# Kernel tuning notes

Hardware: AMD Instinct MI355X
Metric: run time of the kernel (lower is better)

Reference implementation:

```python
import jax, jax.numpy as jnp
import numpy as np
from functools import partial

EPS = 1e-5
TAU = 0.1

def bn(x, g, b, axes):
    m = jnp.mean(x, axis=axes, keepdims=True)
    v = jnp.var(x, axis=axes, keepdims=True)
    return (x - m) * jax.lax.rsqrt(v + EPS) * g + b

def conv(x, w, b):
    # x: NCHW, w: OIHW, stride 1, padding 1
    y = jax.lax.conv_general_dilated(x, w, (1, 1), ((1, 1), (1, 1)),
                                     dimension_numbers=('NCHW', 'OIHW', 'NCHW'))
    return y + b[None, :, None, None]

def maxpool2(x):
    return jax.lax.reduce_window(x, -jnp.inf, jax.lax.max, (1, 1, 2, 2), (1, 1, 2, 2), 'VALID')

def setup_inputs() -> dict:
    key = jax.random.key(0)
    ks = jax.random.split(key, 24)
    s = 0.02
    B = 4096
    d = {}
    d['input_data'] = jax.random.normal(ks[0], (B, 3, 32, 32), jnp.float32)
    d['conv1_w'] = jax.random.normal(ks[1], (32, 3, 3, 3), jnp.float32) * s
    d['conv1_b'] = jnp.zeros((32,), jnp.float32)
    d['bn1_g'] = jnp.ones((32,), jnp.float32); d['bn1_b'] = jnp.zeros((32,), jnp.float32)
    d['conv2_w'] = jax.random.normal(ks[2], (64, 32, 3, 3), jnp.float32) * s
    d['conv2_b'] = jnp.zeros((64,), jnp.float32)
    d['bn2_g'] = jnp.ones((64,), jnp.float32); d['bn2_b'] = jnp.zeros((64,), jnp.float32)
    d['conv3_w'] = jax.random.normal(ks[3], (128, 64, 3, 3), jnp.float32) * s
    d['conv3_b'] = jnp.zeros((128,), jnp.float32)
    d['bn3_g'] = jnp.ones((128,), jnp.float32); d['bn3_b'] = jnp.zeros((128,), jnp.float32)
    d['pre_w'] = jax.random.normal(ks[4], (1024, 8192), jnp.float32) * s
    d['pre_b'] = jnp.zeros((1024,), jnp.float32)
    d['bnp_g'] = jnp.ones((1024,), jnp.float32); d['bnp_b'] = jnp.zeros((1024,), jnp.float32)
    d['disc_w'] = jax.random.normal(ks[5], (384, 1024), jnp.float32) * s
    d['disc_b'] = jnp.zeros((384,), jnp.float32)
    d['bnd_g'] = jnp.ones((384,), jnp.float32); d['bnd_b'] = jnp.zeros((384,), jnp.float32)
    d['dfc_w'] = jax.random.normal(ks[6], (2, 384), jnp.float32) * s
    d['dfc_b'] = jnp.zeros((2,), jnp.float32)
    d['sw_w'] = jax.random.normal(ks[7], (2, 384), jnp.float32) * s
    d['sw_b'] = jnp.zeros((2,), jnp.float32)
    # partitioned classifier: P=2, Linear(1024 -> 192) + ReLU + Linear(192 -> 10)
    d['p1_w'] = jax.random.normal(ks[8], (2, 192, 1024), jnp.float32) * s
    d['p1_b'] = jnp.zeros((2, 192), jnp.float32)
    d['p2_w'] = jax.random.normal(ks[9], (2, 10, 192), jnp.float32) * s
    d['p2_b'] = jnp.zeros((2, 10), jnp.float32)
    return d

def reference(input_data, conv1_w, conv1_b, bn1_g, bn1_b, conv2_w, conv2_b, bn2_g, bn2_b,
              conv3_w, conv3_b, bn3_g, bn3_b, pre_w, pre_b, bnp_g, bnp_b,
              disc_w, disc_b, bnd_g, bnd_b, dfc_w, dfc_b, sw_w, sw_b,
              p1_w, p1_b, p2_w, p2_b):
    B = input_data.shape[0]
    # feature extractor
    x = jax.nn.relu(bn(conv(input_data, conv1_w, conv1_b), bn1_g[None, :, None, None], bn1_b[None, :, None, None], (0, 2, 3)))
    x = maxpool2(x)
    x = jax.nn.relu(bn(conv(x, conv2_w, conv2_b), bn2_g[None, :, None, None], bn2_b[None, :, None, None], (0, 2, 3)))
    x = maxpool2(x)
    x = jax.nn.relu(bn(conv(x, conv3_w, conv3_b), bn3_g[None, :, None, None], bn3_b[None, :, None, None], (0, 2, 3)))
    feat = x.reshape(B, -1)  # [B, 8192]
    feat = jax.nn.relu(bn(feat @ pre_w.T + pre_b, bnp_g[None, :], bnp_b[None, :], (0,)))  # [B, 1024]
    # discriminator branch
    dpen = jax.nn.relu(bn(feat @ disc_w.T + disc_b, bnd_g[None, :], bnd_b[None, :], (0,)))  # [B, 384]
    domain_output = dpen @ dfc_w.T + dfc_b  # [B, 2]
    sw_logits = dpen @ sw_w.T + sw_b  # [B, P]
    # gumbel-softmax (soft) + multinomial sample of partition
    key = jax.random.key(42)
    k1, k2 = jax.random.split(key)
    u = jax.random.uniform(k1, sw_logits.shape, jnp.float32, 1e-10, 1.0)
    gumbel = -jnp.log(-jnp.log(u))
    y = jax.nn.softmax((sw_logits + gumbel) / TAU, axis=-1)  # [B, P]
    partition_idx = jax.random.categorical(k2, jnp.log(y + 1e-20), axis=-1)  # [B]
    # per-partition expert MLP computed densely (P=2), then gather chosen partition
    h = jax.nn.relu(jnp.einsum('bi,poi->pbo', feat, p1_w) + p1_b[:, None, :])  # [P, B, 192]
    logits = jnp.einsum('pbo,pco->pbc', h, p2_w) + p2_b[:, None, :]  # [P, B, 10]
    sel = logits[partition_idx, jnp.arange(B)]  # [B, 10]
    # original multiplies single-element stack by full gumbel vector and sums -> scale by sum(y)=1
    class_output_partitioned = sel * jnp.sum(y, axis=1, keepdims=True)
    return (class_output_partitioned, domain_output, partition_idx)
```

## Files before the change

### kernel.cpp

```cpp
#include <hip/hip_runtime.h>
#include <cstdint>
#include <cstddef>

typedef __attribute__((ext_vector_type(8))) short short8;
typedef __attribute__((ext_vector_type(4))) float f32x4;
typedef __attribute__((ext_vector_type(16))) float f32x16;

__host__ __device__ inline void threefry2x32(uint32_t k0, uint32_t k1,
                                             uint32_t x0, uint32_t x1,
                                             uint32_t& o0, uint32_t& o1) {
  uint32_t ks2 = k0 ^ k1 ^ 0x1BD11BDAu;
  uint32_t v0 = x0 + k0, v1 = x1 + k1;
#define TF_R(r) { v0 += v1; v1 = (v1 << (r)) | (v1 >> (32 - (r))); v1 ^= v0; }
  TF_R(13) TF_R(15) TF_R(26) TF_R(6)
  v0 += k1; v1 += ks2 + 1u;
  TF_R(17) TF_R(29) TF_R(16) TF_R(24)
  v0 += ks2; v1 += k0 + 2u;
  TF_R(13) TF_R(15) TF_R(26) TF_R(6)
  v0 += k0; v1 += k1 + 3u;
  TF_R(17) TF_R(29) TF_R(16) TF_R(24)
  v0 += k1; v1 += ks2 + 4u;
  TF_R(13) TF_R(15) TF_R(26) TF_R(6)
  v0 += ks2; v1 += k0 + 5u;
#undef TF_R
  o0 = v0; o1 = v1;
}

__device__ __forceinline__ uint32_t tf_bits32(uint32_t k0, uint32_t k1, uint32_t j) {
  uint32_t o0, o1;
  threefry2x32(k0, k1, 0u, j, o0, o1);
  return o0 ^ o1;
}

__device__ __forceinline__ float u01_from_bits(uint32_t bits) {
  return __uint_as_float((bits >> 9) | 0x3f800000u) - 1.0f;
}

__device__ __forceinline__ float waveSum(float v) {
#pragma unroll
  for (int off = 32; off > 0; off >>= 1) v += __shfl_down(v, off, 64);
  return v;
}

__global__ __launch_bounds__(256) void conv1_fused_kernel(
    const float* __restrict__ in, const float* __restrict__ w,
    float* __restrict__ outraw, float* __restrict__ partials) {
  __shared__ float ins[3 * 34 * 34];
  __shared__ float red[4][64];
  const int b = blockIdx.x, t = threadIdx.x;
  for (int i = t; i < 3 * 34 * 34; i += 256) {
    int ci = i / 1156, r = i % 1156, iy = r / 34, ix = r % 34;
    int y = iy - 1, x = ix - 1;
    float v = 0.f;
    if ((unsigned)y < 32u && (unsigned)x < 32u)
      v = in[(((size_t)b * 3 + ci) * 32 + y) * 32 + x];
    ins[i] = v;
  }
  __syncthreads();
  const int py = t >> 4, px = t & 15, wv = t >> 6, ln = t & 63;
  float win[3][4][4];
#pragma unroll
  for (int ci = 0; ci < 3; ci++)
#pragma unroll
    for (int r = 0; r < 4; r++)
#pragma unroll
      for (int c = 0; c < 4; c++)
        win[ci][r][c] = ins[ci * 1156 + (2 * py + r) * 34 + (2 * px + c)];
#pragma unroll 1
  for (int co = 0; co < 32; co++) {
    float acc00 = 0.f, acc01 = 0.f, acc10 = 0.f, acc11 = 0.f;
#pragma unroll
    for (int ci = 0; ci < 3; ci++) {
      const float* wp = w + (co * 3 + ci) * 9;
#pragma unroll
      for (int dy = 0; dy < 3; dy++)
#pragma unroll
        for (int dx = 0; dx < 3; dx++) {
          float wvv = wp[dy * 3 + dx];
          acc00 += win[ci][dy][dx] * wvv;
          acc01 += win[ci][dy][dx + 1] * wvv;
          acc10 += win[ci][dy + 1][dx] * wvv;
          acc11 += win[ci][dy + 1][dx + 1] * wvv;
        }
    }
    float sm = acc00 + acc01 + acc10 + acc11;
    float sq = acc00 * acc00 + acc01 * acc01 + acc10 * acc10 + acc11 * acc11;
    float s = waveSum(sm), q = waveSum(sq);
    if (ln == 0) { red[wv][2 * co] = s; red[wv][2 * co + 1] = q; }
    float m = fmaxf(fmaxf(acc00, acc01), fmaxf(acc10, acc11));
    outraw[(((size_t)b * 32 + co) * 16 + py) * 16 + px] = m;
  }
  __syncthreads();
  for (int i = t; i < 64; i += 256)
    partials[(size_t)b * 64 + i] = red[0][i] + red[1][i] + red[2][i] + red[3][i];
}

__device__ __forceinline__ uint32_t pack_bf16q(float x) {
  uint32_t u = __float_as_uint(x);
  uint32_t hi = u & 0xffff0000u;
  float r = x - __uint_as_float(hi);
  uint32_t lo = __float_as_uint(r) >> 16;
  return hi | lo;
}

__device__ __forceinline__ uint4 pk4bn(float4 v, float sc, float sh) {
  uint4 o;
  o.x = pack_bf16q(fmaxf(v.x * sc + sh, 0.f));
  o.y = pack_bf16q(fmaxf(v.y * sc + sh, 0.f));
  o.z = pack_bf16q(fmaxf(v.z * sc + sh, 0.f));
  o.w = pack_bf16q(fmaxf(v.w * sc + sh, 0.f));
  return o;
}

__global__ void cvt_bf16q_kernel(const float* X, uint32_t* Y, int n4) {
  int i = blockIdx.x * blockDim.x + threadIdx.x;
  if (i >= n4) return;
  float4 x = ((const float4*)X)[i];
  uint4 o;
  o.x = pack_bf16q(x.x); o.y = pack_bf16q(x.y);
  o.z = pack_bf16q(x.z); o.w = pack_bf16q(x.w);
  ((uint4*)Y)[i] = o;
}

__global__ void prep_w2_kernel(const float* __restrict__ w, short* __restrict__ wh,
                               short* __restrict__ wl) {
  int idx = blockIdx.x * 256 + threadIdx.x;
  if (idx >= 64 * 32 * 9) return;
  int tp = idx % 9, rem = idx / 9;
  int ci = rem % 32, co = rem / 32;
  uint32_t pq = pack_bf16q(w[idx]);
  size_t o = ((size_t)tp * 64 + co) * 32 + ci;
  wh[o] = (short)(pq >> 16);
  wl[o] = (short)(pq & 0xffffu);
}

__global__ void prep_w3_kernel(const float* __restrict__ w, short* __restrict__ wh,
                               short* __restrict__ wl) {
  int idx = blockIdx.x * 256 + threadIdx.x;
  if (idx >= 128 * 64 * 9) return;
  int tp = idx % 9, rem = idx / 9;
  int ci = rem % 64, co = rem / 64;
  uint32_t pq = pack_bf16q(w[idx]);
  size_t o = ((size_t)tp * 128 + co) * 64 + ci;
  wh[o] = (short)(pq >> 16);
  wl[o] = (short)(pq & 0xffffu);
}

#define STORE2(ARR_H, ARR_L, ROW, KB, SW, U, V)                                 \
  {                                                                             \
    uint32_t h0 = (U.x >> 16) | (U.y & 0xffff0000u);                            \
    uint32_t h1 = (U.z >> 16) | (U.w & 0xffff0000u);                            \
    uint32_t h2 = (V.x >> 16) | (V.y & 0xffff0000u);                            \
    uint32_t h3 = (V.z >> 16) | (V.w & 0xffff0000u);                            \
    uint32_t l0 = (U.x & 0xffffu) | (U.y << 16);                                \
    uint32_t l1 = (U.z & 0xffffu) | (U.w << 16);                                \
    uint32_t l2 = (V.x & 0xffffu) | (V.y << 16);                                \
    uint32_t l3 = (V.z & 0xffffu) | (V.w << 16);                                \
    int idx = (ROW) * 32 + ((KB) ^ (SW));                                       \
    *(uint4*)&ARR_H[idx] = make_uint4(h0, h1, h2, h3);                          \
    *(uint4*)&ARR_L[idx] = make_uint4(l0, l1, l2, l3);                          \
  }

__global__ __launch_bounds__(256) void conv2_mfma_kernel(
    const float* __restrict__ in, const float* __restrict__ scale1,
    const float* __restrict__ shift1, const short* __restrict__ wh,
    const short* __restrict__ wl, float* __restrict__ outpool,
    float* __restrict__ partials) {
  __shared__ short Xh[324 * 32], Xl[324 * 32];
  __shared__ float red[4][128];
  const int b = blockIdx.x, t = threadIdx.x;
  for (int i = t; i < 324 * 16; i += 256) {
    int row = i >> 4;
    int py = row / 18, pxx = row % 18;
    if (py == 0 || py == 17 || pxx == 0 || pxx == 17) {
      ((uint32_t*)Xh)[i] = 0u;
      ((uint32_t*)Xl)[i] = 0u;
    }
  }
  for (int i = t; i < 4096; i += 256) {
    int p = i >> 8, px = i & 255;
    int y = px >> 4, x = px & 15;
    float va = in[((size_t)b * 32 + 2 * p) * 256 + px];
    float vb = in[((size_t)b * 32 + 2 * p + 1) * 256 + px];
    va = fmaxf(va * scale1[2 * p] + shift1[2 * p], 0.f);
    vb = fmaxf(vb * scale1[2 * p + 1] + shift1[2 * p + 1], 0.f);
    uint32_t ua = pack_bf16q(va), ub = pack_bf16q(vb);
    uint32_t h = (ua >> 16) | (ub & 0xffff0000u);
    uint32_t l = (ua & 0xffffu) | (ub << 16);
    int row = (y + 1) * 18 + (x + 1);
    int ci2 = (2 * p) ^ ((row & 3) << 3);
    ((uint32_t*)Xh)[(row * 32 + ci2) >> 1] = h;
    ((uint32_t*)Xl)[(row * 32 + ci2) >> 1] = l;
  }
  __syncthreads();
  const int w = t >> 6, l = t & 63;
  const int lr = l & 15, lg = l >> 4;
  f32x4 acc[4][4];
#pragma unroll
  for (int i = 0; i < 4; i++)
#pragma unroll
    for (int j = 0; j < 4; j++) acc[i][j] = (f32x4){0.f, 0.f, 0.f, 0.f};
#pragma unroll 1
  for (int tap = 0; tap < 9; tap++) {
    const int dy = tap / 3, dx = tap % 3;
    short8 awh[4], awl[4];
#pragma unroll
    for (int i = 0; i < 4; i++) {
      size_t off = ((size_t)tap * 64 + i * 16 + lr) * 32 + lg * 8;
      awh[i] = *(const short8*)(wh + off);
      awl[i] = *(const short8*)(wl + off);
    }
    short8 bxh[4], bxl[4];
#pragma unroll
    for (int j = 0; j < 4; j++) {
      int y = w * 4 + j, x = lr;
      int row = (y + dy) * 18 + (x + dx);
      int ci = (lg * 8) ^ ((row & 3) << 3);
      bxh[j] = *(const short8*)&Xh[row * 32 + ci];
      bxl[j] = *(const short8*)&Xl[row * 32 + ci];
    }
#pragma unroll
    for (int i = 0; i < 4; i++)
#pragma unroll
      for (int j = 0; j < 4; j++) {
        acc[i][j] = __builtin_amdgcn_mfma_f32_16x16x32_bf16(awh[i], bxh[j], acc[i][j], 0, 0, 0);
        acc[i][j] = __builtin_amdgcn_mfma_f32_16x16x32_bf16(awh[i], bxl[j], acc[i][j], 0, 0, 0);
        acc[i][j] = __builtin_amdgcn_mfma_f32_16x16x32_bf16(awl[i], bxh[j], acc[i][j], 0, 0, 0);
      }
  }
#pragma unroll
  for (int i = 0; i < 4; i++)
#pragma unroll
    for (int r = 0; r < 4; r++) {
      int co = i * 16 + lg * 4 + r;
      float v0 = acc[i][0][r], v1 = acc[i][1][r], v2 = acc[i][2][r], v3 = acc[i][3][r];
      float s = v0 + v1 + v2 + v3;
      float q = v0 * v0 + v1 * v1 + v2 * v2 + v3 * v3;
#pragma unroll
      for (int off = 1; off <= 8; off <<= 1) {
        s += __shfl_xor(s, off, 64);
        q += __shfl_xor(q, off, 64);
      }
      if (lr == 0) { red[w][2 * co] = s; red[w][2 * co + 1] = q; }
      float h0 = fmaxf(v0, __shfl_xor(v0, 1, 64));
      float h1 = fmaxf(v1, __shfl_xor(v1, 1, 64));
      float h2 = fmaxf(v2, __shfl_xor(v2, 1, 64));
      float h3 = fmaxf(v3, __shfl_xor(v3, 1, 64));
      float pm0 = fmaxf(h0, h1);
      float pm1 = fmaxf(h2, h3);
      if ((lr & 1) == 0) {
        size_t base = ((size_t)b * 64 + co) * 64 + (w * 2) * 8 + (lr >> 1);
        outpool[base] = pm0;
        outpool[base + 8] = pm1;
      }
    }
  __syncthreads();
  for (int i = t; i < 128; i += 256)
    partials[(size_t)b * 128 + i] = red[0][i] + red[1][i] + red[2][i] + red[3][i];
}

__global__ __launch_bounds__(256) void conv3_mfma_kernel(
    const float* __restrict__ in, const float* __restrict__ scale2,
    const float* __restrict__ shift2, const short* __restrict__ wh,
    const short* __restrict__ wl, float* __restrict__ outraw,
    float* __restrict__ partials) {
  __shared__ short Xh[100 * 64], Xl[100 * 64];
  __shared__ float red[256];
  const int b = blockIdx.x, t = threadIdx.x;
  for (int i = t; i < 100 * 32; i += 256) {
    int row = i >> 5;
    int py = row / 10, pxx = row % 10;
    if (py == 0 || py == 9 || pxx == 0 || pxx == 9) {
      ((uint32_t*)Xh)[i] = 0u;
      ((uint32_t*)Xl)[i] = 0u;
    }
  }
  for (int i = t; i < 2048; i += 256) {
    int p = i >> 6, px = i & 63;
    int y = px >> 3, x = px & 7;
    float va = in[((size_t)b * 64 + 2 * p) * 64 + px];
    float vb = in[((size_t)b * 64 + 2 * p + 1) * 64 + px];
    va = fmaxf(va * scale2[2 * p] + shift2[2 * p], 0.f);
    vb = fmaxf(vb * scale2[2 * p + 1] + shift2[2 * p + 1], 0.f);
    uint32_t ua = pack_bf16q(va), ub = pack_bf16q(vb);
    uint32_t h = (ua >> 16) | (ub & 0xffff0000u);
    uint32_t l = (ua & 0xffffu) | (ub << 16);
    int row = (y + 1) * 10 + (x + 1);
    int ci2 = (2 * p) ^ ((row & 7) << 3);
    ((uint32_t*)Xh)[(row * 64 + ci2) >> 1] = h;
    ((uint32_t*)Xl)[(row * 64 + ci2) >> 1] = l;
  }
  __syncthreads();
  const int w = t >> 6, l = t & 63;
  const int lr = l & 15, lg = l >> 4;
  const int co_base = w * 32;
  f32x4 acc[2][4];
#pragma unroll
  for (int i = 0; i < 2; i++)
#pragma unroll
    for (int j = 0; j < 4; j++) acc[i][j] = (f32x4){0.f, 0.f, 0.f, 0.f};
#pragma unroll 1
  for (int tap = 0; tap < 9; tap++) {
    const int dy = tap / 3, dx = tap % 3;
#pragma unroll
    for (int sl = 0; sl < 2; sl++) {
      short8 awh[2], awl[2];
#pragma unroll
      for (int i = 0; i < 2; i++) {
        size_t off = ((size_t)tap * 128 + co_base + i * 16 + lr) * 64 + sl * 32 + lg * 8;
        awh[i] = *(const short8*)(wh + off);
        awl[i] = *(const short8*)(wl + off);
      }
      short8 bxh[4], bxl[4];
#pragma unroll
      for (int j = 0; j < 4; j++) {
        int px = j * 16 + lr;
        int row = ((px >> 3) + dy) * 10 + (px & 7) + dx;
        int ci = (sl * 32 + lg * 8) ^ ((row & 7) << 3);
        bxh[j] = *(const short8*)&Xh[row * 64 + ci];
        bxl[j] = *(const short8*)&Xl[row * 64 + ci];
      }
#pragma unroll
      for (int i = 0; i < 2; i++)
#pragma unroll
        for (int j = 0; j < 4; j++) {
          acc[i][j] = __builtin_amdgcn_mfma_f32_16x16x32_bf16(awh[i], bxh[j], acc[i][j], 0, 0, 0);
          acc[i][j] = __builtin_amdgcn_mfma_f32_16x16x32_bf16(awh[i], bxl[j], acc[i][j], 0, 0, 0);
          acc[i][j] = __builtin_amdgcn_mfma_f32_16x16x32_bf16(awl[i], bxh[j], acc[i][j], 0, 0, 0);
        }
    }
  }
#pragma unroll
  for (int i = 0; i < 2; i++)
#pragma unroll
    for (int r = 0; r < 4; r++) {
      int co = co_base + i * 16 + lg * 4 + r;
      float s = 0.f, q = 0.f;
#pragma unroll
      for (int j = 0; j < 4; j++) {
        float v = acc[i][j][r];
        outraw[((size_t)b * 128 + co) * 64 + j * 16 + lr] = v;
        s += v; q += v * v;
      }
#pragma unroll
      for (int off = 1; off <= 8; off <<= 1) {
        s += __shfl_xor(s, off, 64);
        q += __shfl_xor(q, off, 64);
      }
      if (lr == 0) { red[2 * co] = s; red[2 * co + 1] = q; }
    }
  __syncthreads();
  for (int i = t; i < 256; i += 256) partials[(size_t)b * 256 + i] = red[i];
}

__global__ __launch_bounds__(256) void reduce_finalize_kernel(
    const float* __restrict__ partials, int nblk, int Q,
    const float* __restrict__ g, const float* __restrict__ b,
    float* __restrict__ scale, float* __restrict__ shift, double invN) {
  int c = blockIdx.x, t = threadIdx.x;
  double s = 0.0, q = 0.0;
  for (int i = t; i < nblk; i += 256) {
    s += (double)partials[(size_t)i * Q + 2 * c];
    q += (double)partials[(size_t)i * Q + 2 * c + 1];
  }
  __shared__ double rs[256], rq[256];
  rs[t] = s; rq[t] = q;
  __syncthreads();
  for (int st = 128; st > 0; st >>= 1) {
    if (t < st) { rs[t] += rs[t + st]; rq[t] += rq[t + st]; }
    __syncthreads();
  }
  if (t == 0) {
    double m = rs[0] * invN;
    double v = rq[0] * invN - m * m;
    double sc = (double)g[c] / sqrt(v + 1e-5);
    scale[c] = (float)sc;
    shift[c] = (float)((double)b[c] - m * sc);
  }
}

__global__ __launch_bounds__(1024) void col_stats_kernel(
    const float* __restrict__ X, const float* __restrict__ Y,
    int R, int C, int nch, double* __restrict__ sums) {
  int c0 = blockIdx.x * 64, chunk = blockIdx.y;
  int cl = threadIdx.x & 63, rg = threadIdx.x >> 6;
  int rows = R / nch, rbeg = chunk * rows, rend = rbeg + rows;
  double s = 0.0, sq = 0.0;
  for (int r = rbeg + rg; r < rend; r += 16) {
    size_t idx = (size_t)r * C + c0 + cl;
    float v = X[idx];
    if (Y) v += Y[idx];
    s += v; sq += (double)v * (double)v;
  }
  __shared__ double red[16][64][2];
  red[rg][cl][0] = s; red[rg][cl][1] = sq;
  __syncthreads();
  if (rg == 0) {
    for (int i = 1; i < 16; i++) { s += red[i][cl][0]; sq += red[i][cl][1]; }
    sums[(size_t)chunk * 2 * C + 2 * (c0 + cl)] = s;
    sums[(size_t)chunk * 2 * C + 2 * (c0 + cl) + 1] = sq;
  }
}

__global__ void bn_finalize_kernel(const double* __restrict__ sums, int nch, int cst2,
                                   const float* __restrict__ g, const float* __restrict__ b,
                                   float* __restrict__ scale, float* __restrict__ shift,
                                   int C, double invN) {
  int c = blockIdx.x * blockDim.x + threadIdx.x;
  if (c >= C) return;
  double s = 0.0, sq = 0.0;
  for (int ch = 0; ch < nch; ch++) {
    s += sums[(size_t)ch * cst2 + 2 * c];
    sq += sums[(size_t)ch * cst2 + 2 * c + 1];
  }
  double m = s * invN;
  double v = sq * invN - m * m;
  double sc = (double)g[c] / sqrt(v + 1e-5);
  scale[c] = (float)sc;
  shift[c] = (float)((double)b[c] - m * sc);
}

__global__ void bn_relu_pack_cols4_kernel(float* __restrict__ X,
                                          const float* __restrict__ Y,
                                          const float* __restrict__ scale,
                                          const float* __restrict__ shift,
                                          int n4, int C4) {
  int i = blockIdx.x * blockDim.x + threadIdx.x;
  if (i >= n4) return;
  int c4 = i % C4;
  float4 v = ((float4*)X)[i];
  if (Y) {
    float4 y = ((const float4*)Y)[i];
    v.x += y.x; v.y += y.y; v.z += y.z; v.w += y.w;
  }
  float4 sc = ((const float4*)scale)[c4];
  float4 sh = ((const float4*)shift)[c4];
  uint4 o;
  o.x = pack_bf16q(fmaxf(v.x * sc.x + sh.x, 0.f));
  o.y = pack_bf16q(fmaxf(v.y * sc.y + sh.y, 0.f));
  o.z = pack_bf16q(fmaxf(v.z * sc.z + sh.z, 0.f));
  o.w = pack_bf16q(fmaxf(v.w * sc.w + sh.w, 0.f));
  ((uint4*)X)[i] = o;
}

__global__ void bn_relu_cols4_kernel(float* __restrict__ X, const float* __restrict__ scale,
                                     const float* __restrict__ shift, int n4, int C4) {
  int i = blockIdx.x * blockDim.x + threadIdx.x;
  if (i >= n4) return;
  int c4 = i % C4;
  float4 v = ((float4*)X)[i];
  float4 sc = ((const float4*)scale)[c4];
  float4 sh = ((const float4*)shift)[c4];
  v.x = fmaxf(v.x * sc.x + sh.x, 0.f);
  v.y = fmaxf(v.y * sc.y + sh.y, 0.f);
  v.z = fmaxf(v.z * sc.z + sh.z, 0.f);
  v.w = fmaxf(v.w * sc.w + sh.w, 0.f);
  ((float4*)X)[i] = v;
}

__device__ __forceinline__ int swz16(int row) {
  return ((row & 3) ^ ((row >> 2) & 3)) << 3;
}

__global__ __launch_bounds__(256) void gemm_bf16q_dual_kernel(
    const uint32_t* __restrict__ A, const uint32_t* __restrict__ B0,
    const uint32_t* __restrict__ B1, const float* __restrict__ bias1,
    float* __restrict__ C0, float* __restrict__ C1, int M, int N, int K) {
  __shared__ short Ah[128 * 32], Al[128 * 32], Bh[64 * 32], Bl[64 * 32];
  const int t = threadIdx.x;
  const int nTN = N >> 6;
  const int tiles = (M >> 7) * nTN;
  const int half = (blockIdx.x >= tiles) ? 1 : 0;
  const uint32_t* B = half ? B1 : B0;
  float* C = half ? C1 : C0;
  const int bid = blockIdx.x - half * tiles;
  const int mPer = (M >> 7) >> 3;
  const int xcd = bid & 7, qq = bid >> 3;
  const int m0 = (xcd * mPer + qq / nTN) << 7;
  const int n0 = (qq % nTN) << 6;
  const int w = t >> 6, l = t & 63;
  const int wrow = (w >> 1) << 6, wcol = (w & 1) << 5;
  const int lr = l & 15, lg = l >> 4;
  const int ar = t >> 1, akh = (t & 1) << 4;
  const int br = t >> 2, bkh = (t & 3) << 3;
  const int asw = swz16(ar), bsw = swz16(br);
  const uint32_t* Ap = A + (size_t)(m0 + ar) * K + akh;
  const uint32_t* Bp = B + (size_t)(n0 + br) * K + bkh;
  f32x4 acc[4][2];
#pragma unroll
  for (int i = 0; i < 4; i++)
#pragma unroll
    for (int j = 0; j < 2; j++) acc[i][j] = (f32x4){0.f, 0.f, 0.f, 0.f};
  uint4 ra0 = *(const uint4*)(Ap + 0), ra1 = *(const uint4*)(Ap + 4);
  uint4 ra2 = *(const uint4*)(Ap + 8), ra3 = *(const uint4*)(Ap + 12);
  uint4 rb0 = *(const uint4*)(Bp + 0), rb1 = *(const uint4*)(Bp + 4);
  const int NS = K >> 5;
  for (int s = 0; s < NS; s++) {
    __syncthreads();
    STORE2(Ah, Al, ar, akh + 0, asw, ra0, ra1)
    STORE2(Ah, Al, ar, akh + 8, asw, ra2, ra3)
    STORE2(Bh, Bl, br, bkh, bsw, rb0, rb1)
    __syncthreads();
    if (s + 1 < NS) {
      int ko = (s + 1) << 5;
      ra0 = *(const uint4*)(Ap + ko); ra1 = *(const uint4*)(Ap + ko + 4);
      ra2 = *(const uint4*)(Ap + ko + 8); ra3 = *(const uint4*)(Ap + ko + 12);
      rb0 = *(const uint4*)(Bp + ko); rb1 = *(const uint4*)(Bp + ko + 4);
    }
    short8 ahf[4], alf[4], bhf[2], blf[2];
#pragma unroll
    for (int i = 0; i < 4; i++) {
      int R = wrow + i * 16 + lr;
      int kk = (lg << 3) ^ swz16(R);
      ahf[i] = *(const short8*)&Ah[R * 32 + kk];
      alf[i] = *(const short8*)&Al[R * 32 + kk];
    }
#pragma unroll
    for (int j = 0; j < 2; j++) {
      int Cc = wcol + j * 16 + lr;
      int kk = (lg << 3) ^ swz16(Cc);
      bhf[j] = *(const short8*)&Bh[Cc * 32 + kk];
      blf[j] = *(const short8*)&Bl[Cc * 32 + kk];
    }
#pragma unroll
    for (int i = 0; i < 4; i++)
#pragma unroll
      for (int j = 0; j < 2; j++) {
        acc[i][j] = __builtin_amdgcn_mfma_f32_16x16x32_bf16(ahf[i], bhf[j], acc[i][j], 0, 0, 0);
        acc[i][j] = __builtin_amdgcn_mfma_f32_16x16x32_bf16(ahf[i], blf[j], acc[i][j], 0, 0, 0);
        acc[i][j] = __builtin_amdgcn_mfma_f32_16x16x32_bf16(alf[i], bhf[j], acc[i][j], 0, 0, 0);
      }
  }
#pragma unroll
  for (int i = 0; i < 4; i++)
#pragma unroll
    for (int j = 0; j < 2; j++) {
      int n = n0 + wcol + j * 16 + lr;
#pragma unroll
      for (int r = 0; r < 4; r++) {
        int m = m0 + wrow + i * 16 + lg * 4 + r;
        float v = acc[i][j][r];
        if (half) v = fmaxf(v + bias1[n], 0.f);
        C[(size_t)m * N + n] = v;
      }
    }
}

__global__ __launch_bounds__(256, 2) void gemm_bf16q_big_kernel(
    const float* __restrict__ A, const uint32_t* __restrict__ B,
    const float* __restrict__ scale, const float* __restrict__ shift,
    float* __restrict__ C0, float* __restrict__ C1, int M, int N, int K) {
  __shared__ short Ah[2][128 * 32], Al[2][128 * 32], Bh[2][128 * 32], Bl[2][128 * 32];
  const int t = threadIdx.x;
  const int nTN = N >> 7;
  const int tiles = (M >> 7) * nTN;
  const int mPer = (M >> 7) >> 3;
  const int split = blockIdx.x / tiles;
  const int bid = blockIdx.x % tiles;
  const int xcd = bid & 7, qq = bid >> 3;
  const int m0 = (xcd * mPer + qq / nTN) << 7;
  const int n0 = (qq % nTN) << 7;
  const int Kh = K >> 1;
  const int kbeg = split * Kh;
  float* Cout = split ? C1 : C0;
  const int w = t >> 6, l = t & 63;
  const int wrow = (w & 1) << 6, wcol = (w >> 1) << 6;
  const int l31 = l & 31, lg2 = l >> 5;
  const int ar = t >> 1, akh = (t & 1) << 4;
  const int asw = swz16(ar);
  const float* Ap = A + (size_t)(m0 + ar) * K + kbeg + akh;
  const uint32_t* Bp = B + (size_t)(n0 + ar) * K + kbeg + akh;
  f32x16 acc[2][2];
#pragma unroll
  for (int i = 0; i < 2; i++)
#pragma unroll
    for (int j = 0; j < 2; j++)
#pragma unroll
      for (int r = 0; r < 16; r++) acc[i][j][r] = 0.f;
  const int NS = Kh >> 5;
  float4 fa0 = *(const float4*)(Ap + 0), fa1 = *(const float4*)(Ap + 4);
  float4 fa2 = *(const float4*)(Ap + 8), fa3 = *(const float4*)(Ap + 12);
  uint4 rb0 = *(const uint4*)(Bp + 0), rb1 = *(const uint4*)(Bp + 4);
  uint4 rb2 = *(const uint4*)(Bp + 8), rb3 = *(const uint4*)(Bp + 12);
  {
    int ch = (kbeg + akh) >> 6;
    float sc = scale[ch], sh = shift[ch];
    uint4 ua0 = pk4bn(fa0, sc, sh), ua1 = pk4bn(fa1, sc, sh);
    uint4 ua2 = pk4bn(fa2, sc, sh), ua3 = pk4bn(fa3, sc, sh);
    STORE2(Ah[0], Al[0], ar, akh + 0, asw, ua0, ua1)
    STORE2(Ah[0], Al[0], ar, akh + 8, asw, ua2, ua3)
    STORE2(Bh[0], Bl[0], ar, akh + 0, asw, rb0, rb1)
    STORE2(Bh[0], Bl[0], ar, akh + 8, asw, rb2, rb3)
  }
  if (NS > 1) {
    fa0 = *(const float4*)(Ap + 32); fa1 = *(const float4*)(Ap + 36);
    fa2 = *(const float4*)(Ap + 40); fa3 = *(const float4*)(Ap + 44);
    rb0 = *(const uint4*)(Bp + 32); rb1 = *(const uint4*)(Bp + 36);
    rb2 = *(const uint4*)(Bp + 40); rb3 = *(const uint4*)(Bp + 44);
  }
  __syncthreads();
  int cur = 0;
  for (int s = 0; s < NS; s++) {
    short8 ahf[2][2], alf[2][2], bhf[2][2], blf[2][2];
#pragma unroll
    for (int fi = 0; fi < 2; fi++)
#pragma unroll
      for (int kh = 0; kh < 2; kh++) {
        int R = wrow + fi * 32 + l31;
        int kk = (lg2 * 8 + kh * 16) ^ swz16(R);
        ahf[fi][kh] = *(const short8*)&Ah[cur][R * 32 + kk];
        alf[fi][kh] = *(const short8*)&Al[cur][R * 32 + kk];
      }
#pragma unroll
    for (int fj = 0; fj < 2; fj++)
#pragma unroll
      for (int kh = 0; kh < 2; kh++) {
        int Cc = wcol + fj * 32 + l31;
        int kk = (lg2 * 8 + kh * 16) ^ swz16(Cc);
        bhf[fj][kh] = *(const short8*)&Bh[cur][Cc * 32 + kk];
        blf[fj][kh] = *(const short8*)&Bl[cur][Cc * 32 + kk];
      }
    if (s + 1 < NS) {
      int nxt = cur ^ 1;
      int ch = (kbeg + akh + ((s + 1) << 5)) >> 6;
      float sc = scale[ch], sh = shift[ch];
      uint4 ua0 = pk4bn(fa0, sc, sh), ua1 = pk4bn(fa1, sc, sh);
      uint4 ua2 = pk4bn(fa2, sc, sh), ua3 = pk4bn(fa3, sc, sh);
      STORE2(Ah[nxt], Al[nxt], ar, akh + 0, asw, ua0, ua1)
      STORE2(Ah[nxt], Al[nxt], ar, akh + 8, asw, ua2, ua3)
      STORE2(Bh[nxt], Bl[nxt], ar, akh + 0, asw, rb0, rb1)
      STORE2(Bh[nxt], Bl[nxt], ar, akh + 8, asw, rb2, rb3)
      if (s + 2 < NS) {
        int ko = (s + 2) << 5;
        fa0 = *(const float4*)(Ap + ko); fa1 = *(const float4*)(Ap + ko + 4);
        fa2 = *(const float4*)(Ap + ko + 8); fa3 = *(const float4*)(Ap + ko + 12);
        rb0 = *(const uint4*)(Bp + ko); rb1 = *(const uint4*)(Bp + ko + 4);
        rb2 = *(const uint4*)(Bp + ko + 8); rb3 = *(const uint4*)(Bp + ko + 12);
      }
    }
#pragma unroll
    for (int fi = 0; fi < 2; fi++)
#pragma unroll
      for (int fj = 0; fj < 2; fj++)
#pragma unroll
        for (int kh = 0; kh < 2; kh++) {
          acc[fi][fj] = __builtin_amdgcn_mfma_f32_32x32x16_bf16(ahf[fi][kh], bhf[fj][kh], acc[fi][fj], 0, 0, 0);
          acc[fi][fj] = __builtin_amdgcn_mfma_f32_32x32x16_bf16(ahf[fi][kh], blf[fj][kh], acc[fi][fj], 0, 0, 0);
          acc[fi][fj] = __builtin_amdgcn_mfma_f32_32x32x16_bf16(alf[fi][kh], bhf[fj][kh], acc[fi][fj], 0, 0, 0);
        }
    __syncthreads();
    cur ^= 1;
  }
#pragma unroll
  for (int fi = 0; fi < 2; fi++)
#pragma unroll
    for (int fj = 0; fj < 2; fj++) {
      int n = n0 + wcol + fj * 32 + l31;
#pragma unroll
      for (int r = 0; r < 16; r++) {
        int m = m0 + wrow + fi * 32 + (r & 3) + 8 * (r >> 2) + 4 * lg2;
        Cout[(size_t)m * N + n] = acc[fi][fj][r];
      }
    }
}

__global__ __launch_bounds__(256) void heads_kernel(
    const float* __restrict__ dpen, const float* __restrict__ dfc_w,
    const float* __restrict__ dfc_b, const float* __restrict__ sw_w,
    const float* __restrict__ sw_b, float* __restrict__ out_dom,
    float* __restrict__ swbuf) {
  int wv = threadIdx.x >> 6, ln = threadIdx.x & 63;
  int b = blockIdx.x * 4 + wv;
  const float* row = dpen + (size_t)b * 384;
  double a0 = 0.0, a1 = 0.0, a2 = 0.0, a3 = 0.0;
  for (int k = ln; k < 384; k += 64) {
    double rv = (double)row[k];
    a0 += rv * (double)dfc_w[k];
    a1 += rv * (double)dfc_w[384 + k];
    a2 += rv * (double)sw_w[k];
    a3 += rv * (double)sw_w[384 + k];
  }
#pragma unroll
  for (int off = 32; off > 0; off >>= 1) {
    a0 += __shfl_down(a0, off, 64);
    a1 += __shfl_down(a1, off, 64);
    a2 += __shfl_down(a2, off, 64);
    a3 += __shfl_down(a3, off, 64);
  }
  if (ln == 0) {
    out_dom[b * 2 + 0] = (float)(a0 + (double)dfc_b[0]);
    out_dom[b * 2 + 1] = (float)(a1 + (double)dfc_b[1]);
    swbuf[b * 2 + 0] = (float)(a2 + (double)sw_b[0]);
    swbuf[b * 2 + 1] = (float)(a3 + (double)sw_b[1]);
  }
}

__global__ __launch_bounds__(256) void partition_kernel(
    const float* __restrict__ swbuf, float* __restrict__ out_pid,
    int* __restrict__ pidxI, float* __restrict__ ysum,
    uint32_t k1a, uint32_t k1b, uint32_t k2a, uint32_t k2b) {
  int b = blockIdx.x * 256 + threadIdx.x;
  if (b >= 4096) return;
  uint32_t j0 = (uint32_t)(2 * b), j1 = (uint32_t)(2 * b + 1);
  float f0 = u01_from_bits(tf_bits32(k1a, k1b, j0));
  float f1 = u01_from_bits(tf_bits32(k1a, k1b, j1));
  const float MINV = 1e-10f;
  float u0 = fmaxf(MINV, f0 * (1.0f - MINV) + MINV);
  float u1 = fmaxf(MINV, f1 * (1.0f - MINV) + MINV);
  double g0 = -log(-log((double)u0));
  double g1 = -log(-log((double)u1));
  double s0 = (double)swbuf[2 * b], s1 = (double)swbuf[2 * b + 1];
  double x0 = (s0 + g0) / 0.1;
  double x1 = (s1 + g1) / 0.1;
  double mx = fmax(x0, x1);
  double e0 = exp(x0 - mx), e1 = exp(x1 - mx);
  double es = e0 + e1;
  double y0 = e0 / es, y1 = e1 / es;
  float h0 = u01_from_bits(tf_bits32(k2a, k2b, j0));
  float h1 = u01_from_bits(tf_bits32(k2a, k2b, j1));
  const float TINY = 1.17549435e-38f;
  float v0 = fmaxf(TINY, h0 * (1.0f - TINY) + TINY);
  float v1 = fmaxf(TINY, h1 * (1.0f - TINY) + TINY);
  double gg0 = -log(-log((double)v0));
  double gg1 = -log(-log((double)v1));
  double l0 = log(y0 + 1e-20) + gg0;
  double l1 = log(y1 + 1e-20) + gg1;
  int p = (l1 > l0) ? 1 : 0;
  out_pid[b] = (float)p;
  pidxI[b] = p;
  ysum[b] = (float)(y0 + y1);
}

__global__ __launch_bounds__(256) void final_kernel(
    const float* __restrict__ h, const float* __restrict__ p2w,
    const float* __restrict__ p2b, const int* __restrict__ pidxI,
    const float* __restrict__ ysum, float* __restrict__ out0) {
  int t = blockIdx.x * 256 + threadIdx.x;
  if (t >= 40960) return;
  int b = t / 10, c = t % 10;
  int p = pidxI[b];
  const float* hr = h + (size_t)b * 384 + p * 192;
  const float* wr = p2w + ((size_t)p * 10 + c) * 192;
  float s = 0.f;
  for (int o = 0; o < 192; o++) s += hr[o] * wr[o];
  s += p2b[p * 10 + c];
  out0[t] = s * ysum[b];
}

extern "C" void kernel_launch(void* const* d_in, const int* in_sizes, int n_in,
                              void* d_out, int out_size, void* d_ws, size_t ws_size,
                              hipStream_t stream) {
  const float* input   = (const float*)d_in[0];
  const float* conv1_w = (const float*)d_in[1];
  const float* bn1_g   = (const float*)d_in[3];
  const float* bn1_b   = (const float*)d_in[4];
  const float* conv2_w = (const float*)d_in[5];
  const float* bn2_g   = (const float*)d_in[7];
  const float* bn2_b   = (const float*)d_in[8];
  const float* conv3_w = (const float*)d_in[9];
  const float* bn3_g   = (const float*)d_in[11];
  const float* bn3_b   = (const float*)d_in[12];
  const float* pre_w   = (const float*)d_in[13];
  const float* bnp_g   = (const float*)d_in[15];
  const float* bnp_b   = (const float*)d_in[16];
  const float* disc_w  = (const float*)d_in[17];
  const float* bnd_g   = (const float*)d_in[19];
  const float* bnd_b   = (const float*)d_in[20];
  const float* dfc_w   = (const float*)d_in[21];
  const float* dfc_b   = (const float*)d_in[22];
  const float* sw_w    = (const float*)d_in[23];
  const float* sw_b    = (const float*)d_in[24];
  const float* p1_w    = (const float*)d_in[25];
  const float* p1_b    = (const float*)d_in[26];
  const float* p2_w    = (const float*)d_in[27];
  const float* p2_b    = (const float*)d_in[28];

  float* W = (float*)d_ws;
  float* pool1  = W + 0;
  float* pool2  = W + 33554432;
  float* act3   = W + 0;
  uint32_t* Bcvt = (uint32_t*)(W + 33554432);
  uint32_t* discq = (uint32_t*)(W + 41943040);
  uint32_t* p1q   = (uint32_t*)(W + 42336256);
  float* csplit = W + 42729472;
  float* featp  = W + 50331648;
  uint32_t* featq = (uint32_t*)featp;
  short* wh3    = (short*)(W + 50331648);
  short* wl3    = (short*)(W + 50368512);
  short* wh2    = (short*)(W + 50405376);
  short* wl2    = (short*)(W + 50414592);
  float* dpen   = W + 54525952;
  float* hbuf   = W + 56098816;
  float* swbuf  = W + 57671680;
  float* ysum   = W + 57679872;
  int*   pidxI  = (int*)(W + 57683968);
  float* part   = W + 57688064;
  double* sums  = (double*)(W + 58736640);
  float* scale  = W + 58769408;
  float* shift  = W + 58770432;

  float* out_cls = (float*)d_out;
  float* out_dom = out_cls + 40960;
  float* out_pid = out_cls + 49152;

  uint32_t k1a, k1b, k2a, k2b;
  threefry2x32(0u, 42u, 0u, 0u, k1a, k1b);
  threefry2x32(0u, 42u, 0u, 1u, k2a, k2b);

  conv1_fused_kernel<<<dim3(4096), dim3(256), 0, stream>>>(input, conv1_w, pool1, part);
  reduce_finalize_kernel<<<dim3(32), dim3(256), 0, stream>>>(part, 4096, 64, bn1_g, bn1_b, scale, shift, 1.0 / (4096.0 * 1024.0));

  prep_w2_kernel<<<dim3(72), dim3(256), 0, stream>>>(conv2_w, wh2, wl2);
  conv2_mfma_kernel<<<dim3(4096), dim3(256), 0, stream>>>(pool1, scale, shift, wh2, wl2, pool2, part);
  reduce_finalize_kernel<<<dim3(64), dim3(256), 0, stream>>>(part, 4096, 128, bn2_g, bn2_b, scale, shift, 1.0 / (4096.0 * 256.0));

  prep_w3_kernel<<<dim3(288), dim3(256), 0, stream>>>(conv3_w, wh3, wl3);
  conv3_mfma_kernel<<<dim3(4096), dim3(256), 0, stream>>>(pool2, scale, shift, wh3, wl3, act3, part);
  reduce_finalize_kernel<<<dim3(128), dim3(256), 0, stream>>>(part, 4096, 256, bn3_g, bn3_b, scale, shift, 1.0 / (4096.0 * 64.0));

  cvt_bf16q_kernel<<<dim3(8192), dim3(256), 0, stream>>>(pre_w, Bcvt, 2097152);
  gemm_bf16q_big_kernel<<<dim3(512), dim3(256), 0, stream>>>(act3, Bcvt, scale, shift, featp, csplit, 4096, 1024, 8192);
  col_stats_kernel<<<dim3(16, 8), dim3(1024), 0, stream>>>(featp, csplit, 4096, 1024, 8, sums);
  bn_finalize_kernel<<<dim3(4), dim3(256), 0, stream>>>(sums, 8, 2048, bnp_g, bnp_b, scale, shift, 1024, 1.0 / 4096.0);
  bn_relu_pack_cols4_kernel<<<dim3(4096), dim3(256), 0, stream>>>(featp, csplit, scale, shift, 1048576, 256);

  cvt_bf16q_kernel<<<dim3(384), dim3(256), 0, stream>>>(disc_w, discq, 98304);
  cvt_bf16q_kernel<<<dim3(384), dim3(256), 0, stream>>>(p1_w, p1q, 98304);
  gemm_bf16q_dual_kernel<<<dim3(384), dim3(256), 0, stream>>>(featq, discq, p1q, p1_b, dpen, hbuf, 4096, 384, 1024);
  col_stats_kernel<<<dim3(6, 8), dim3(1024), 0, stream>>>(dpen, (const float*)nullptr, 4096, 384, 8, sums);
  bn_finalize_kernel<<<dim3(2), dim3(256), 0, stream>>>(sums, 8, 768, bnd_g, bnd_b, scale, shift, 384, 1.0 / 4096.0);
  bn_relu_cols4_kernel<<<dim3(1536), dim3(256), 0, stream>>>(dpen, scale, shift, 393216, 96);

  heads_kernel<<<dim3(1024), dim3(256), 0, stream>>>(dpen, dfc_w, dfc_b, sw_w, sw_b, out_dom, swbuf);
  partition_kernel<<<dim3(16), dim3(256), 0, stream>>>(swbuf, out_pid, pidxI, ysum, k1a, k1b, k2a, k2b);

  final_kernel<<<dim3(160), dim3(256), 0, stream>>>(hbuf, p2_w, p2_b, pidxI, ysum, out_cls);
}
```

Before: 834.4 us.

## Load B fragments directly from global memory into registers, bypassing LDS

The quantized-GEMM kernel stops staging the packed B tile in shared memory. Each lane now loads its B fragment directly from global memory at every k-step and splits it into hi/lo bf16 halves in registers. This removes the B LDS stores and reads and halves shared memory use, which could allow more resident blocks. In exchange, the B loads are no longer prefetched a step ahead, and waves that share columns fetch the same data redundantly, so global latency may be exposed.

Result: slower. 969.2 us (+16.2%).

```diff
diff --git a/kernel.cpp b/kernel.cpp
--- a/kernel.cpp
+++ b/kernel.cpp
@@ -550,7 +550,7 @@
     const float* __restrict__ A, const uint32_t* __restrict__ B,
     const float* __restrict__ scale, const float* __restrict__ shift,
     float* __restrict__ C0, float* __restrict__ C1, int M, int N, int K) {
-  __shared__ short Ah[2][128 * 32], Al[2][128 * 32], Bh[2][128 * 32], Bl[2][128 * 32];
+  __shared__ short Ah[2][128 * 32], Al[2][128 * 32];
   const int t = threadIdx.x;
   const int nTN = N >> 7;
   const int tiles = (M >> 7) * nTN;
@@ -569,7 +569,6 @@
   const int ar = t >> 1, akh = (t & 1) << 4;
   const int asw = swz16(ar);
   const float* Ap = A + (size_t)(m0 + ar) * K + kbeg + akh;
-  const uint32_t* Bp = B + (size_t)(n0 + ar) * K + kbeg + akh;
   f32x16 acc[2][2];
 #pragma unroll
   for (int i = 0; i < 2; i++)
@@ -580,8 +579,6 @@
   const int NS = Kh >> 5;
   float4 fa0 = *(const float4*)(Ap + 0), fa1 = *(const float4*)(Ap + 4);
   float4 fa2 = *(const float4*)(Ap + 8), fa3 = *(const float4*)(Ap + 12);
-  uint4 rb0 = *(const uint4*)(Bp + 0), rb1 = *(const uint4*)(Bp + 4);
-  uint4 rb2 = *(const uint4*)(Bp + 8), rb3 = *(const uint4*)(Bp + 12);
   {
     int ch = (kbeg + akh) >> 6;
     float sc = scale[ch], sh = shift[ch];
@@ -589,19 +586,25 @@
     uint4 ua2 = pk4bn(fa2, sc, sh), ua3 = pk4bn(fa3, sc, sh);
     STORE2(Ah[0], Al[0], ar, akh + 0, asw, ua0, ua1)
     STORE2(Ah[0], Al[0], ar, akh + 8, asw, ua2, ua3)
-    STORE2(Bh[0], Bl[0], ar, akh + 0, asw, rb0, rb1)
-    STORE2(Bh[0], Bl[0], ar, akh + 8, asw, rb2, rb3)
   }
   if (NS > 1) {
     fa0 = *(const float4*)(Ap + 32); fa1 = *(const float4*)(Ap + 36);
     fa2 = *(const float4*)(Ap + 40); fa3 = *(const float4*)(Ap + 44);
-    rb0 = *(const uint4*)(Bp + 32); rb1 = *(const uint4*)(Bp + 36);
-    rb2 = *(const uint4*)(Bp + 40); rb3 = *(const uint4*)(Bp + 44);
   }
   __syncthreads();
   int cur = 0;
   for (int s = 0; s < NS; s++) {
-    short8 ahf[2][2], alf[2][2], bhf[2][2], blf[2][2];
+    uint4 bq[2][2][2];
+#pragma unroll
+    for (int fj = 0; fj < 2; fj++)
+#pragma unroll
+      for (int kh = 0; kh < 2; kh++) {
+        size_t boff = (size_t)(n0 + wcol + fj * 32 + l31) * K +
+                      (size_t)(kbeg + (s << 5) + lg2 * 8 + kh * 16);
+        bq[fj][kh][0] = *(const uint4*)(B + boff);
+        bq[fj][kh][1] = *(const uint4*)(B + boff + 4);
+      }
+    short8 ahf[2][2], alf[2][2];
 #pragma unroll
     for (int fi = 0; fi < 2; fi++)
 #pragma unroll
@@ -610,15 +613,6 @@
         int kk = (lg2 * 8 + kh * 16) ^ swz16(R);
         ahf[fi][kh] = *(const short8*)&Ah[cur][R * 32 + kk];
         alf[fi][kh] = *(const short8*)&Al[cur][R * 32 + kk];
-      }
-#pragma unroll
-    for (int fj = 0; fj < 2; fj++)
-#pragma unroll
-      for (int kh = 0; kh < 2; kh++) {
-        int Cc = wcol + fj * 32 + l31;
-        int kk = (lg2 * 8 + kh * 16) ^ swz16(Cc);
-        bhf[fj][kh] = *(const short8*)&Bh[cur][Cc * 32 + kk];
-        blf[fj][kh] = *(const short8*)&Bl[cur][Cc * 32 + kk];
       }
     if (s + 1 < NS) {
       int nxt = cur ^ 1;
@@ -628,16 +622,30 @@
       uint4 ua2 = pk4bn(fa2, sc, sh), ua3 = pk4bn(fa3, sc, sh);
       STORE2(Ah[nxt], Al[nxt], ar, akh + 0, asw, ua0, ua1)
       STORE2(Ah[nxt], Al[nxt], ar, akh + 8, asw, ua2, ua3)
-      STORE2(Bh[nxt], Bl[nxt], ar, akh + 0, asw, rb0, rb1)
-      STORE2(Bh[nxt], Bl[nxt], ar, akh + 8, asw, rb2, rb3)
       if (s + 2 < NS) {
         int ko = (s + 2) << 5;
         fa0 = *(const float4*)(Ap + ko); fa1 = *(const float4*)(Ap + ko + 4);
         fa2 = *(const float4*)(Ap + ko + 8); fa3 = *(const float4*)(Ap + ko + 12);
-        rb0 = *(const uint4*)(Bp + ko); rb1 = *(const uint4*)(Bp + ko + 4);
-        rb2 = *(const uint4*)(Bp + ko + 8); rb3 = *(const uint4*)(Bp + ko + 12);
-      }
-    }
+      }
+    }
+    short8 bhf[2][2], blf[2][2];
+#pragma unroll
+    for (int fj = 0; fj < 2; fj++)
+#pragma unroll
+      for (int kh = 0; kh < 2; kh++) {
+        uint4 u = bq[fj][kh][0], v = bq[fj][kh][1];
+        union { uint32_t q[4]; short8 s8; } H, L;
+        H.q[0] = (u.x >> 16) | (u.y & 0xffff0000u);
+        H.q[1] = (u.z >> 16) | (u.w & 0xffff0000u);
+        H.q[2] = (v.x >> 16) | (v.y & 0xffff0000u);
+        H.q[3] = (v.z >> 16) | (v.w & 0xffff0000u);
+        L.q[0] = (u.x & 0xffffu) | (u.y << 16);
+        L.q[1] = (u.z & 0xffffu) | (u.w << 16);
+        L.q[2] = (v.x & 0xffffu) | (v.y << 16);
+        L.q[3] = (v.z & 0xffffu) | (v.w << 16);
+        bhf[fj][kh] = H.s8;
+        blf[fj][kh] = L.s8;
+      }
 #pragma unroll
     for (int fi = 0; fi < 2; fi++)
 #pragma unroll
```
